# Optimization experiments

Hardware: AMD Instinct MI355X
Metric: run time of the kernel (lower is better)

Reference implementation:

```python
import jax, jax.numpy as jnp
import numpy as np

NUM_HEADS = 16
ROPE_THETA = 10000.0


def setup_inputs() -> dict:
    key = jax.random.key(0)
    k1, k2, k3 = jax.random.split(key, 3)
    B, S, D = 2, 2048, 1024
    std_qkv = float(np.sqrt(2.0 / (D + 3 * D)))
    std_out = float(np.sqrt(2.0 / (D + D)))
    return {
        "x": jax.random.normal(k1, (B, S, D), dtype=jnp.float32),
        "qkv_w": jax.random.normal(k2, (3 * D, D), dtype=jnp.float32) * std_qkv,
        "out_w": jax.random.normal(k3, (D, D), dtype=jnp.float32) * std_out,
        "token_positions": jnp.arange(S, dtype=jnp.int32),
    }


def _apply_rope(x, token_positions, theta=ROPE_THETA):
    # x: [B, H, S, d_k], token_positions: [S]
    d_k = x.shape[-1]
    inv_freqs = 1.0 / (theta ** (jnp.arange(0, d_k, 2, dtype=jnp.float32) / d_k))  # [d_k/2]
    angles = token_positions.astype(jnp.float32)[:, None] * inv_freqs[None, :]     # [S, d_k/2]
    cos, sin = jnp.cos(angles), jnp.sin(angles)
    x_even, x_odd = x[..., 0::2], x[..., 1::2]
    r_even = x_even * cos - x_odd * sin
    r_odd = x_even * sin + x_odd * cos
    # interleave back: [..., d_k/2, 2] -> [..., d_k]
    return jnp.stack([r_even, r_odd], axis=-1).reshape(x.shape)


def reference(x, qkv_w, out_w, token_positions):
    B, S, D = x.shape
    H = NUM_HEADS
    d_k = D // H

    qkv = jnp.einsum("bsd,ed->bse", x, qkv_w)                  # [B, S, 3*D]
    qkv = qkv.reshape(B, S, 3, H, d_k)
    q, k, v = (jnp.transpose(qkv[:, :, i], (0, 2, 1, 3)) for i in range(3))  # each [B, H, S, d_k]

    q = _apply_rope(q, token_positions)
    k = _apply_rope(k, token_positions)

    scale = 1.0 / jnp.sqrt(jnp.asarray(d_k, dtype=x.dtype))
    scores = jnp.einsum("bhqd,bhkd->bhqk", q, k) * scale       # [B, H, S, S]
    causal = jnp.tril(jnp.ones((S, S), dtype=bool))
    scores = jnp.where(causal, scores, jnp.asarray(-jnp.inf, dtype=scores.dtype))
    attn = jax.nn.softmax(scores, axis=-1)
    out = jnp.einsum("bhqk,bhkd->bhqd", attn, v)               # [B, H, S, d_k]
    out = jnp.transpose(out, (0, 2, 1, 3)).reshape(B, S, D)    # [B, S, D]
    return jnp.einsum("bsd,ed->bse", out, out_w)               # [B, S, D]
```

## Files before the change

### kernel.cpp

```cpp
#include <hip/hip_runtime.h>

typedef __bf16 bf16x8 __attribute__((ext_vector_type(8)));
typedef float f32x4 __attribute__((ext_vector_type(4)));
typedef unsigned short u16;
typedef u16 u16x8 __attribute__((ext_vector_type(8)));
typedef u16 u16x4 __attribute__((ext_vector_type(4)));
typedef u16 u16x2 __attribute__((ext_vector_type(2)));

__device__ __forceinline__ u16 f2bf(float f) {
    union { float f; unsigned u; } x; x.f = f;
    unsigned r = x.u + 0x7fffu + ((x.u >> 16) & 1u);
    return (u16)(r >> 16);
}
__device__ __forceinline__ float bf2f(u16 v) {
    union { unsigned u; float f; } x; x.u = ((unsigned)v) << 16;
    return x.f;
}
__device__ __forceinline__ bf16x8 as_bf16x8(u16x8 v) {
    return __builtin_bit_cast(bf16x8, v);
}
__device__ __forceinline__ void glds16(const void* g, void* l) {
    __builtin_amdgcn_global_load_lds(
        (const __attribute__((address_space(1))) void*)g,
        (__attribute__((address_space(3))) void*)l, 16, 0, 0);
}
__device__ __forceinline__ int swz(int r) { return (((r & 7) ^ ((r >> 3) & 7)) << 3); }

__global__ __launch_bounds__(256) void cvt3(const float* __restrict__ x,
                                            const float* __restrict__ w,
                                            const float* __restrict__ ow,
                                            u16* __restrict__ x16,
                                            u16* __restrict__ w16,
                                            u16* __restrict__ ow16) {
    int i = blockIdx.x * 256 + threadIdx.x;
    const float* in; u16* out; int off;
    if (i < 524288)       { in = x;  out = x16;  off = i; }
    else if (i < 917504)  { in = w;  out = w16;  off = i - 524288; }
    else                  { in = ow; out = ow16; off = i - 917504; }
    const float4* p = (const float4*)(in + (size_t)off * 8);
    float4 a = p[0], b = p[1];
    u16x8 o;
    o[0] = f2bf(a.x); o[1] = f2bf(a.y); o[2] = f2bf(a.z); o[3] = f2bf(a.w);
    o[4] = f2bf(b.x); o[5] = f2bf(b.y); o[6] = f2bf(b.z); o[7] = f2bf(b.w);
    *(u16x8*)(out + (size_t)off * 8) = o;
}

__global__ __launch_bounds__(256) void gemm_qkv(const u16* __restrict__ A,
                                                const u16* __restrict__ B,
                                                u16* __restrict__ Qb,
                                                u16* __restrict__ Kb,
                                                u16* __restrict__ Vt) {
    __shared__ u16 smem[17408];
    const int K = 1024, nbx = 24;
    const int tid = threadIdx.x, lane = tid & 63, wave = tid >> 6;
    const int cpx = gridDim.x >> 3;
    const int nid = (blockIdx.x & 7) * cpx + (blockIdx.x >> 3);
    const int m0 = (nid / nbx) << 7, n0 = (nid % nbx) << 7;
    const int wr = (wave >> 1) << 6, wc = (wave & 1) << 6;
    const int fr = lane & 15, fo = (lane >> 4) << 3;
    const int srow = tid >> 2, scol = (tid & 3) << 3;
    const u16* Ag = A + (size_t)(m0 + srow) * K + scol;
    const u16* Bg = B + (size_t)(n0 + srow) * K + scol;
    u16* AsW = smem + (wave << 9);
    u16* BsW = smem + 8192 + (wave << 9);
    f32x4 acc[4][4] = {};
    const int nsteps = K >> 5;
    glds16(Ag, AsW);
    glds16(Ag + (size_t)64 * K, AsW + 2048);
    glds16(Bg, BsW);
    glds16(Bg + (size_t)64 * K, BsW + 2048);
    int cur = 0;
    for (int s = 0; s < nsteps; ++s) {
        __syncthreads();
        if (s + 1 < nsteps) {
            const u16* Ap = Ag + (s + 1) * 32;
            const u16* Bp = Bg + (s + 1) * 32;
            const int nb = (cur ^ 1) << 12;
            glds16(Ap, AsW + nb);
            glds16(Ap + (size_t)64 * K, AsW + nb + 2048);
            glds16(Bp, BsW + nb);
            glds16(Bp + (size_t)64 * K, BsW + nb + 2048);
        }
        const u16* Ab = smem + (cur << 12);
        const u16* Bb = smem + 8192 + (cur << 12);
        bf16x8 af[4], bfr[4];
        #pragma unroll
        for (int i = 0; i < 4; ++i)
            af[i] = *(const bf16x8*)(Ab + (wr + i * 16 + fr) * 32 + fo);
        #pragma unroll
        for (int i = 0; i < 4; ++i)
            bfr[i] = *(const bf16x8*)(Bb + (wc + i * 16 + fr) * 32 + fo);
        #pragma unroll
        for (int i = 0; i < 4; ++i)
            #pragma unroll
            for (int j = 0; j < 4; ++j)
                acc[i][j] = __builtin_amdgcn_mfma_f32_16x16x32_bf16(af[i], bfr[j], acc[i][j], 0, 0, 0);
        cur ^= 1;
    }
    const int cr = (lane >> 4) << 2, cc = lane & 15;
    const int bb = m0 >> 11, sb = m0 & 2047;
    __syncthreads();
    if (n0 >= 2048) {
        #pragma unroll
        for (int i = 0; i < 4; ++i) {
            const int sl = wr + i * 16 + cr;
            const int k = sl & 63;
            const int p0 = ((sl >> 6) << 6) + ((k >> 5) << 5) + (((k >> 2) & 3) << 3)
                         + (((k >> 4) & 1) << 2);
            #pragma unroll
            for (int j = 0; j < 4; ++j) {
                const int c = wc + j * 16 + cc;
                u16x4 v4;
                #pragma unroll
                for (int r = 0; r < 4; ++r) v4[r] = f2bf(acc[i][j][r]);
                *(u16x4*)&smem[c * 136 + p0] = v4;
            }
        }
        __syncthreads();
        const int c = tid >> 1, hf = tid & 1;
        const int hh = c >> 6, d = c & 63;
        const int h0 = (n0 - 2048) >> 6;
        u16* dst = Vt + (((size_t)(bb * 16 + h0 + hh)) << 17) + ((size_t)d << 11)
                 + sb + (hf << 6);
        const u16* sr = &smem[c * 136 + (hf << 6)];
        #pragma unroll
        for (int q = 0; q < 8; ++q)
            *(u16x8*)(dst + q * 8) = *(const u16x8*)(sr + q * 8);
    } else {
        const bool isQ = (n0 < 1024);
        const float qs = isQ ? 0.18033688011112042f : 1.0f;
        const float sgn = (cc & 1) ? 1.f : -1.f;
        #pragma unroll
        for (int j = 0; j < 4; ++j) {
            const int c = wc + j * 16 + cc;
            const int tr = (c & 63) >> 1;
            const float invf = exp2f((float)tr * -0.4152410118609203f)
                             * 0.15915494309189535f;
            #pragma unroll
            for (int i = 0; i < 4; ++i) {
                #pragma unroll
                for (int r = 0; r < 4; ++r) {
                    const int sl = wr + i * 16 + cr + r;
                    float own  = acc[i][j][r];
                    float part = __shfl_xor(own, 1);
                    float rev  = (float)(sb + sl) * invf;
                    rev -= floorf(rev);
                    float sn = __builtin_amdgcn_sinf(rev);
                    float cs = __builtin_amdgcn_cosf(rev);
                    smem[sl * 136 + c] = f2bf((cs * own + sgn * sn * part) * qs);
                }
            }
        }
        __syncthreads();
        const int sl = tid >> 1, hh = tid & 1;
        const int h0 = (isQ ? n0 : (n0 - 1024)) >> 6;
        u16* Outb = isQ ? Qb : Kb;
        u16* dst = Outb + (((size_t)(bb * 16 + h0 + hh)) << 17)
                 + ((size_t)(sb + sl) << 6);
        const u16* sr = &smem[sl * 136 + (hh << 6)];
        #pragma unroll
        for (int q = 0; q < 8; ++q)
            *(u16x8*)(dst + q * 8) = *(const u16x8*)(sr + q * 8);
    }
}

template<bool BF16OUT>
__global__ __launch_bounds__(256) void gemm128(const u16* __restrict__ A,
                                               const u16* __restrict__ B,
                                               void* __restrict__ Cv,
                                               int N, int K, int nbx) {
    __shared__ u16 As[2][4096];
    __shared__ u16 Bs[2][4096];
    const int tid = threadIdx.x, lane = tid & 63, wave = tid >> 6;
    const int cpx = gridDim.x >> 3;
    const int nid = (blockIdx.x & 7) * cpx + (blockIdx.x >> 3);
    const int m0 = (nid / nbx) << 7, n0 = (nid % nbx) << 7;
    const int wr = (wave >> 1) << 6, wc = (wave & 1) << 6;
    const int fr = lane & 15, fo = (lane >> 4) << 3;
    const int srow = tid >> 2, scol = (tid & 3) << 3;
    const u16* Ag = A + (size_t)(m0 + srow) * K + scol;
    const u16* Bg = B + (size_t)(n0 + srow) * K + scol;
    u16* AsW = &As[0][0] + (wave << 9);
    u16* BsW = &Bs[0][0] + (wave << 9);
    f32x4 acc[4][4] = {};
    const int nsteps = K >> 5;
    glds16(Ag, AsW);
    glds16(Ag + (size_t)64 * K, AsW + 2048);
    glds16(Bg, BsW);
    glds16(Bg + (size_t)64 * K, BsW + 2048);
    int cur = 0;
    for (int s = 0; s < nsteps; ++s) {
        __syncthreads();
        if (s + 1 < nsteps) {
            const u16* Ap = Ag + (s + 1) * 32;
            const u16* Bp = Bg + (s + 1) * 32;
            const int nb = (cur ^ 1) << 12;
            glds16(Ap, AsW + nb);
            glds16(Ap + (size_t)64 * K, AsW + nb + 2048);
            glds16(Bp, BsW + nb);
            glds16(Bp + (size_t)64 * K, BsW + nb + 2048);
        }
        const u16* Ab = &As[cur][0];
        const u16* Bb = &Bs[cur][0];
        bf16x8 af[4], bfr[4];
        #pragma unroll
        for (int i = 0; i < 4; ++i)
            af[i] = *(const bf16x8*)(Ab + (wr + i * 16 + fr) * 32 + fo);
        #pragma unroll
        for (int i = 0; i < 4; ++i)
            bfr[i] = *(const bf16x8*)(Bb + (wc + i * 16 + fr) * 32 + fo);
        #pragma unroll
        for (int i = 0; i < 4; ++i)
            #pragma unroll
            for (int j = 0; j < 4; ++j)
                acc[i][j] = __builtin_amdgcn_mfma_f32_16x16x32_bf16(af[i], bfr[j], acc[i][j], 0, 0, 0);
        cur ^= 1;
    }
    const int cr = (lane >> 4) << 2, cc = lane & 15;
    if constexpr (BF16OUT) {
        u16* C = (u16*)Cv;
        #pragma unroll
        for (int i = 0; i < 4; ++i)
            for (int j = 0; j < 4; ++j)
                for (int r = 0; r < 4; ++r)
                    C[(size_t)(m0 + wr + i * 16 + cr + r) * N + (n0 + wc + j * 16 + cc)] =
                        f2bf(acc[i][j][r]);
    } else {
        float* C = (float*)Cv;
        #pragma unroll
        for (int i = 0; i < 4; ++i)
            for (int j = 0; j < 4; ++j)
                for (int r = 0; r < 4; ++r)
                    C[(size_t)(m0 + wr + i * 16 + cr + r) * N + (n0 + wc + j * 16 + cc)] =
                        acc[i][j][r];
    }
}

__global__ __launch_bounds__(512, 4) void attn_causal(const u16* __restrict__ Q,
                                                      const u16* __restrict__ K,
                                                      const u16* __restrict__ Vt,
                                                      u16* __restrict__ O) {
    __shared__ u16 smem[24576];
    __shared__ float cmb[5120];
    const int tid = threadIdx.x, lane = tid & 63, wave = tid >> 6;
    const int nid = ((blockIdx.x & 7) << 6) + (blockIdx.x >> 3);
    const int pr = nid & 15, h = (nid >> 4) & 15, b = nid >> 8;
    const int S = 2048;
    const size_t base = (size_t)((b << 4) + h) << 17;
    const int fr = lane & 15, fo = (lane >> 4) << 3, cr = (lane >> 4) << 2;
    const int schk = lane & 7, srow8 = lane >> 3;
    const int qsub = wave >> 1, half = wave & 1;
    float* const slot = cmb + qsub * 1280 + lane * 20;
    u16x8 ones_u;
    #pragma unroll
    for (int i = 0; i < 8; ++i) ones_u[i] = 0x3F80;
    const bf16x8 ones = as_bf16x8(ones_u);

    auto stage = [&](int t, int bi) {
        const int r  = (wave << 3) + srow8;
        const int ck = (schk ^ srow8 ^ wave) << 3;
        glds16(K  + base + ((size_t)((t << 6) + r) << 6) + ck,
               &smem[bi * 8192 + (wave << 9)]);
        glds16(Vt + base + ((size_t)r << 11) + (t << 6) + ck,
               &smem[bi * 8192 + 4096 + (wave << 9)]);
    };

    for (int phase = 0; phase < 2; ++phase) {
        const int qt = phase ? (31 - pr) : pr;
        const int nkt = qt + 1;
        const int qw = (qt << 6) + (qsub << 4);
        bf16x8 aq0, aq1;
        {
            const u16* qrow = Q + base + (size_t)(qw + fr) * 64;
            aq0 = as_bf16x8(*(const u16x8*)(qrow + fo));
            aq1 = as_bf16x8(*(const u16x8*)(qrow + 32 + fo));
        }
        f32x4 oacc[4] = {};
        f32x4 lacc = {};
        const int qloc = (qsub << 4) + fr;
        stage(0, 0);
        if (nkt > 1) stage(1, 1);
        int cur = 0;
        for (int t = 0; t < nkt; ++t) {
            if (t + 1 < nkt) asm volatile("s_waitcnt vmcnt(2)" ::: "memory");
            else             asm volatile("s_waitcnt vmcnt(0)" ::: "memory");
            __builtin_amdgcn_s_barrier();
            __builtin_amdgcn_sched_barrier(0);
            int nb = cur + 2; if (nb >= 3) nb -= 3;
            if (t + 2 < nkt) stage(t + 2, nb);
            const u16* Kb = smem + cur * 8192;
            const u16* Vb = smem + cur * 8192 + 4096;
            const bool diag = (t == nkt - 1);
            f32x4 sacc[2];
            __builtin_amdgcn_s_setprio(1);
            #pragma unroll
            for (int ch = 0; ch < 2; ++ch) {
                const int r = ((half << 1) + ch) * 16 + fr;
                const int sw = swz(r);
                bf16x8 bk0 = *(const bf16x8*)&Kb[r * 64 + (fo ^ sw)];
                bf16x8 bk1 = *(const bf16x8*)&Kb[r * 64 + ((32 + fo) ^ sw)];
                f32x4 sc = {};
                sc = __builtin_amdgcn_mfma_f32_16x16x32_bf16(bk0, aq0, sc, 0, 0, 0);
                sc = __builtin_amdgcn_mfma_f32_16x16x32_bf16(bk1, aq1, sc, 0, 0, 0);
                sacc[ch] = sc;
            }
            __builtin_amdgcn_s_setprio(0);
            bf16x8 pa;
            #pragma unroll
            for (int ch = 0; ch < 2; ++ch) {
                const int cglob = (half << 1) + ch;
                #pragma unroll
                for (int r = 0; r < 4; ++r) {
                    float e = exp2f(sacc[ch][r]);
                    if (diag) {
                        const int kloc = (cglob << 4) + cr + r;
                        e = (kloc <= qloc) ? e : 0.f;
                    }
                    pa[ch * 4 + r] = (__bf16)e;
                }
            }
            __builtin_amdgcn_s_setprio(1);
            lacc = __builtin_amdgcn_mfma_f32_16x16x32_bf16(pa, ones, lacc, 0, 0, 0);
            #pragma unroll
            for (int tt = 0; tt < 4; ++tt) {
                const int d = tt * 16 + fr;
                bf16x8 bv = *(const bf16x8*)&Vb[d * 64 + (((half << 5) + fo) ^ swz(d))];
                oacc[tt] = __builtin_amdgcn_mfma_f32_16x16x32_bf16(pa, bv, oacc[tt], 0, 0, 0);
            }
            __builtin_amdgcn_s_setprio(0);
            cur = (cur + 1 == 3) ? 0 : cur + 1;
        }
        __syncthreads();
        if (half) {
            #pragma unroll
            for (int tt = 0; tt < 4; ++tt) *(f32x4*)(slot + tt * 4) = oacc[tt];
            *(f32x4*)(slot + 16) = lacc;
        }
        __syncthreads();
        if (!half) {
            #pragma unroll
            for (int tt = 0; tt < 4; ++tt) oacc[tt] += *(const f32x4*)(slot + tt * 4);
            lacc += *(const f32x4*)(slot + 16);
            f32x4 inv;
            #pragma unroll
            for (int j = 0; j < 4; ++j) inv[j] = 1.f / lacc[j];
            #pragma unroll
            for (int tt = 0; tt < 4; ++tt)
                for (int j = 0; j < 4; ++j)
                    O[(size_t)(b * S + qw + cr + j) * 1024 + h * 64 + tt * 16 + fr] =
                        f2bf(oacc[tt][j] * inv[j]);
        }
        __syncthreads();
    }
}

extern "C" void kernel_launch(void* const* d_in, const int* in_sizes, int n_in,
                              void* d_out, int out_size, void* d_ws, size_t ws_size,
                              hipStream_t stream) {
    const float* x     = (const float*)d_in[0];
    const float* qkv_w = (const float*)d_in[1];
    const float* out_w = (const float*)d_in[2];
    float* out = (float*)d_out;

    char* ws = (char*)d_ws;
    u16* Qb    = (u16*)(ws + 25165824);
    u16* Kb    = (u16*)(ws + 33554432);
    u16* Vtg   = (u16*)(ws + 41943040);
    u16* x16   = (u16*)(ws + 50331648);
    u16* att16 = (u16*)(ws + 50331648);
    u16* w16   = (u16*)(ws + 58720256);
    u16* ow16  = (u16*)(ws + 65011712);

    cvt3<<<4096, 256, 0, stream>>>(x, qkv_w, out_w, x16, w16, ow16);
    gemm_qkv<<<768, 256, 0, stream>>>(x16, w16, Qb, Kb, Vtg);
    attn_causal<<<512, 512, 0, stream>>>(Qb, Kb, Vtg, att16);
    gemm128<false><<<256, 256, 0, stream>>>(att16, ow16, (void*)out, 1024, 1024, 8);
}
```

Before: 115.4 us.

## Switch attention to 32x32x16 MFMA with 4 waves and 32-row query tiles

Rewrites the causal attention inner loop to use 32x32x16 bf16 MFMA instead of 16x16x32. Each block now runs 4 waves (256 threads, two per query half), each wave covering 32 query rows and 32 keys, and K/V staging is widened to two loads per wave. The larger MFMA tile is meant to cut LDS operand reads per flop and issue overhead. In exchange it needs more accumulator registers, does a two-step LDS reduction of the output, and changes the V-transpose store permutation in the QKV GEMM epilogue, which could break the layout if it does not match the new reads.

Result: slower. 118.8 us (+2.9%).

```diff
diff --git a/kernel.cpp b/kernel.cpp
--- a/kernel.cpp
+++ b/kernel.cpp
@@ -2,19 +2,15 @@
 
 typedef __bf16 bf16x8 __attribute__((ext_vector_type(8)));
 typedef float f32x4 __attribute__((ext_vector_type(4)));
+typedef float f32x16 __attribute__((ext_vector_type(16)));
 typedef unsigned short u16;
 typedef u16 u16x8 __attribute__((ext_vector_type(8)));
 typedef u16 u16x4 __attribute__((ext_vector_type(4)));
-typedef u16 u16x2 __attribute__((ext_vector_type(2)));
 
 __device__ __forceinline__ u16 f2bf(float f) {
     union { float f; unsigned u; } x; x.f = f;
     unsigned r = x.u + 0x7fffu + ((x.u >> 16) & 1u);
     return (u16)(r >> 16);
-}
-__device__ __forceinline__ float bf2f(u16 v) {
-    union { unsigned u; float f; } x; x.u = ((unsigned)v) << 16;
-    return x.f;
 }
 __device__ __forceinline__ bf16x8 as_bf16x8(u16x8 v) {
     return __builtin_bit_cast(bf16x8, v);
@@ -105,16 +101,19 @@
         for (int i = 0; i < 4; ++i) {
             const int sl = wr + i * 16 + cr;
             const int k = sl & 63;
-            const int p0 = ((sl >> 6) << 6) + ((k >> 5) << 5) + (((k >> 2) & 3) << 3)
-                         + (((k >> 4) & 1) << 2);
+            const int p0 = ((sl >> 6) << 6)
+                         + (k & ~12) | 0;
+            const int ps = (((sl >> 6) << 6) + (k & ~12))
+                         + ((cr & 4) << 1) + ((cr & 8) >> 1);
             #pragma unroll
             for (int j = 0; j < 4; ++j) {
                 const int c = wc + j * 16 + cc;
                 u16x4 v4;
                 #pragma unroll
                 for (int r = 0; r < 4; ++r) v4[r] = f2bf(acc[i][j][r]);
-                *(u16x4*)&smem[c * 136 + p0] = v4;
-            }
+                *(u16x4*)&smem[c * 136 + ps] = v4;
+            }
+            (void)p0;
         }
         __syncthreads();
         const int c = tid >> 1, hf = tid & 1;
@@ -164,10 +163,9 @@
     }
 }
 
-template<bool BF16OUT>
 __global__ __launch_bounds__(256) void gemm128(const u16* __restrict__ A,
                                                const u16* __restrict__ B,
-                                               void* __restrict__ Cv,
+                                               float* __restrict__ C,
                                                int N, int K, int nbx) {
     __shared__ u16 As[2][4096];
     __shared__ u16 Bs[2][4096];
@@ -217,138 +215,157 @@
         cur ^= 1;
     }
     const int cr = (lane >> 4) << 2, cc = lane & 15;
-    if constexpr (BF16OUT) {
-        u16* C = (u16*)Cv;
-        #pragma unroll
-        for (int i = 0; i < 4; ++i)
-            for (int j = 0; j < 4; ++j)
-                for (int r = 0; r < 4; ++r)
-                    C[(size_t)(m0 + wr + i * 16 + cr + r) * N + (n0 + wc + j * 16 + cc)] =
-                        f2bf(acc[i][j][r]);
-    } else {
-        float* C = (float*)Cv;
-        #pragma unroll
-        for (int i = 0; i < 4; ++i)
-            for (int j = 0; j < 4; ++j)
-                for (int r = 0; r < 4; ++r)
-                    C[(size_t)(m0 + wr + i * 16 + cr + r) * N + (n0 + wc + j * 16 + cc)] =
-                        acc[i][j][r];
-    }
-}
-
-__global__ __launch_bounds__(512, 4) void attn_causal(const u16* __restrict__ Q,
+    #pragma unroll
+    for (int i = 0; i < 4; ++i)
+        for (int j = 0; j < 4; ++j)
+            for (int r = 0; r < 4; ++r)
+                C[(size_t)(m0 + wr + i * 16 + cr + r) * N + (n0 + wc + j * 16 + cc)] =
+                    acc[i][j][r];
+}
+
+__global__ __launch_bounds__(256, 2) void attn_causal(const u16* __restrict__ Q,
                                                       const u16* __restrict__ K,
                                                       const u16* __restrict__ Vt,
                                                       u16* __restrict__ O) {
     __shared__ u16 smem[24576];
-    __shared__ float cmb[5120];
+    __shared__ float cmb[4224];
     const int tid = threadIdx.x, lane = tid & 63, wave = tid >> 6;
     const int nid = ((blockIdx.x & 7) << 6) + (blockIdx.x >> 3);
     const int pr = nid & 15, h = (nid >> 4) & 15, b = nid >> 8;
-    const int S = 2048;
     const size_t base = (size_t)((b << 4) + h) << 17;
-    const int fr = lane & 15, fo = (lane >> 4) << 3, cr = (lane >> 4) << 2;
+    const int lq = lane & 31, hi = lane >> 5;
     const int schk = lane & 7, srow8 = lane >> 3;
-    const int qsub = wave >> 1, half = wave & 1;
-    float* const slot = cmb + qsub * 1280 + lane * 20;
+    const int qh = wave >> 1, kh = wave & 1;
+    float* const slot = cmb + (qh * 64 + lane) * 33;
     u16x8 ones_u;
     #pragma unroll
     for (int i = 0; i < 8; ++i) ones_u[i] = 0x3F80;
     const bf16x8 ones = as_bf16x8(ones_u);
 
     auto stage = [&](int t, int bi) {
-        const int r  = (wave << 3) + srow8;
-        const int ck = (schk ^ srow8 ^ wave) << 3;
-        glds16(K  + base + ((size_t)((t << 6) + r) << 6) + ck,
-               &smem[bi * 8192 + (wave << 9)]);
-        glds16(Vt + base + ((size_t)r << 11) + (t << 6) + ck,
-               &smem[bi * 8192 + 4096 + (wave << 9)]);
+        #pragma unroll
+        for (int g = 0; g < 2; ++g) {
+            const int rg = (wave << 4) + (g << 3);
+            const int r  = rg + srow8;
+            const int ck = (schk ^ srow8 ^ ((2 * wave + g) & 7)) << 3;
+            glds16(K  + base + ((size_t)((t << 6) + r) << 6) + ck,
+                   &smem[bi * 8192 + (rg << 6)]);
+            glds16(Vt + base + ((size_t)r << 11) + (t << 6) + ck,
+                   &smem[bi * 8192 + 4096 + (rg << 6)]);
+        }
     };
 
     for (int phase = 0; phase < 2; ++phase) {
         const int qt = phase ? (31 - pr) : pr;
         const int nkt = qt + 1;
-        const int qw = (qt << 6) + (qsub << 4);
-        bf16x8 aq0, aq1;
+        const int qw = (qt << 6) + (qh << 5);
+        const int qg = qw + lq;
+        bf16x8 aq[4];
         {
-            const u16* qrow = Q + base + (size_t)(qw + fr) * 64;
-            aq0 = as_bf16x8(*(const u16x8*)(qrow + fo));
-            aq1 = as_bf16x8(*(const u16x8*)(qrow + 32 + fo));
-        }
-        f32x4 oacc[4] = {};
-        f32x4 lacc = {};
-        const int qloc = (qsub << 4) + fr;
+            const u16* qrow = Q + base + ((size_t)qg << 6) + (hi << 3);
+            #pragma unroll
+            for (int m = 0; m < 4; ++m)
+                aq[m] = as_bf16x8(*(const u16x8*)(qrow + m * 16));
+        }
+        f32x16 oacc0 = {}, oacc1 = {}, lacc = {};
         stage(0, 0);
         if (nkt > 1) stage(1, 1);
         int cur = 0;
         for (int t = 0; t < nkt; ++t) {
-            if (t + 1 < nkt) asm volatile("s_waitcnt vmcnt(2)" ::: "memory");
+            if (t + 1 < nkt) asm volatile("s_waitcnt vmcnt(4)" ::: "memory");
             else             asm volatile("s_waitcnt vmcnt(0)" ::: "memory");
             __builtin_amdgcn_s_barrier();
             __builtin_amdgcn_sched_barrier(0);
             int nb = cur + 2; if (nb >= 3) nb -= 3;
             if (t + 2 < nkt) stage(t + 2, nb);
             const u16* Kb = smem + cur * 8192;
-            const u16* Vb = smem + cur * 8192 + 4096;
+            const u16* Vb = Kb + 4096;
             const bool diag = (t == nkt - 1);
-            f32x4 sacc[2];
+            f32x16 sacc = {};
             __builtin_amdgcn_s_setprio(1);
-            #pragma unroll
-            for (int ch = 0; ch < 2; ++ch) {
-                const int r = ((half << 1) + ch) * 16 + fr;
-                const int sw = swz(r);
-                bf16x8 bk0 = *(const bf16x8*)&Kb[r * 64 + (fo ^ sw)];
-                bf16x8 bk1 = *(const bf16x8*)&Kb[r * 64 + ((32 + fo) ^ sw)];
-                f32x4 sc = {};
-                sc = __builtin_amdgcn_mfma_f32_16x16x32_bf16(bk0, aq0, sc, 0, 0, 0);
-                sc = __builtin_amdgcn_mfma_f32_16x16x32_bf16(bk1, aq1, sc, 0, 0, 0);
-                sacc[ch] = sc;
+            {
+                const int krow = (kh << 5) + lq;
+                const int sw = swz(krow);
+                #pragma unroll
+                for (int m = 0; m < 4; ++m) {
+                    bf16x8 bk = *(const bf16x8*)&Kb[krow * 64 +
+                                                    (((m << 4) + (hi << 3)) ^ sw)];
+                    sacc = __builtin_amdgcn_mfma_f32_32x32x16_bf16(bk, aq[m], sacc, 0, 0, 0);
+                }
             }
             __builtin_amdgcn_s_setprio(0);
-            bf16x8 pa;
-            #pragma unroll
-            for (int ch = 0; ch < 2; ++ch) {
-                const int cglob = (half << 1) + ch;
-                #pragma unroll
-                for (int r = 0; r < 4; ++r) {
-                    float e = exp2f(sacc[ch][r]);
-                    if (diag) {
-                        const int kloc = (cglob << 4) + cr + r;
-                        e = (kloc <= qloc) ? e : 0.f;
-                    }
-                    pa[ch * 4 + r] = (__bf16)e;
-                }
+            bf16x8 pa0, pa1;
+            #pragma unroll
+            for (int r = 0; r < 8; ++r) {
+                float e = exp2f(sacc[r]);
+                if (diag) {
+                    const int kgl = (t << 6) + (kh << 5) + (r & 3) + ((r >> 2) << 3) + (hi << 2);
+                    e = (kgl <= qg) ? e : 0.f;
+                }
+                pa0[r] = (__bf16)e;
+            }
+            #pragma unroll
+            for (int r = 0; r < 8; ++r) {
+                float e = exp2f(sacc[8 + r]);
+                if (diag) {
+                    const int kgl = (t << 6) + (kh << 5) + 16 + (r & 3) + ((r >> 2) << 3) + (hi << 2);
+                    e = (kgl <= qg) ? e : 0.f;
+                }
+                pa1[r] = (__bf16)e;
             }
             __builtin_amdgcn_s_setprio(1);
-            lacc = __builtin_amdgcn_mfma_f32_16x16x32_bf16(pa, ones, lacc, 0, 0, 0);
-            #pragma unroll
-            for (int tt = 0; tt < 4; ++tt) {
-                const int d = tt * 16 + fr;
-                bf16x8 bv = *(const bf16x8*)&Vb[d * 64 + (((half << 5) + fo) ^ swz(d))];
-                oacc[tt] = __builtin_amdgcn_mfma_f32_16x16x32_bf16(pa, bv, oacc[tt], 0, 0, 0);
+            lacc = __builtin_amdgcn_mfma_f32_32x32x16_bf16(pa0, ones, lacc, 0, 0, 0);
+            lacc = __builtin_amdgcn_mfma_f32_32x32x16_bf16(pa1, ones, lacc, 0, 0, 0);
+            #pragma unroll
+            for (int dn = 0; dn < 2; ++dn) {
+                const int vrow = (dn << 5) + lq;
+                const int sw = swz(vrow);
+                bf16x8 bv0 = *(const bf16x8*)&Vb[vrow * 64 +
+                                                 (((kh << 5) + (hi << 3)) ^ sw)];
+                bf16x8 bv1 = *(const bf16x8*)&Vb[vrow * 64 +
+                                                 (((kh << 5) + 16 + (hi << 3)) ^ sw)];
+                if (dn == 0) {
+                    oacc0 = __builtin_amdgcn_mfma_f32_32x32x16_bf16(pa0, bv0, oacc0, 0, 0, 0);
+                    oacc0 = __builtin_amdgcn_mfma_f32_32x32x16_bf16(pa1, bv1, oacc0, 0, 0, 0);
+                } else {
+                    oacc1 = __builtin_amdgcn_mfma_f32_32x32x16_bf16(pa0, bv0, oacc1, 0, 0, 0);
+                    oacc1 = __builtin_amdgcn_mfma_f32_32x32x16_bf16(pa1, bv1, oacc1, 0, 0, 0);
+                }
             }
             __builtin_amdgcn_s_setprio(0);
             cur = (cur + 1 == 3) ? 0 : cur + 1;
         }
         __syncthreads();
-        if (half) {
-            #pragma unroll
-            for (int tt = 0; tt < 4; ++tt) *(f32x4*)(slot + tt * 4) = oacc[tt];
-            *(f32x4*)(slot + 16) = lacc;
-        }
-        __syncthreads();
-        if (!half) {
-            #pragma unroll
-            for (int tt = 0; tt < 4; ++tt) oacc[tt] += *(const f32x4*)(slot + tt * 4);
-            lacc += *(const f32x4*)(slot + 16);
-            f32x4 inv;
-            #pragma unroll
-            for (int j = 0; j < 4; ++j) inv[j] = 1.f / lacc[j];
-            #pragma unroll
-            for (int tt = 0; tt < 4; ++tt)
-                for (int j = 0; j < 4; ++j)
-                    O[(size_t)(b * S + qw + cr + j) * 1024 + h * 64 + tt * 16 + fr] =
-                        f2bf(oacc[tt][j] * inv[j]);
+        if (kh) {
+            #pragma unroll
+            for (int r = 0; r < 16; ++r) slot[r] = oacc0[r];
+            #pragma unroll
+            for (int r = 0; r < 16; ++r) slot[16 + r] = lacc[r];
+        }
+        __syncthreads();
+        if (!kh) {
+            #pragma unroll
+            for (int r = 0; r < 16; ++r) oacc0[r] += slot[r];
+            #pragma unroll
+            for (int r = 0; r < 16; ++r) lacc[r] += slot[16 + r];
+        }
+        __syncthreads();
+        if (kh) {
+            #pragma unroll
+            for (int r = 0; r < 16; ++r) slot[r] = oacc1[r];
+        }
+        __syncthreads();
+        if (!kh) {
+            #pragma unroll
+            for (int r = 0; r < 16; ++r) oacc1[r] += slot[r];
+            #pragma unroll
+            for (int r = 0; r < 16; ++r) {
+                const int q = qw + (r & 3) + ((r >> 2) << 3) + (hi << 2);
+                const float iv = 1.f / lacc[r];
+                u16* op = O + ((size_t)((b << 11) + q) << 10) + (h << 6) + lq;
+                op[0]  = f2bf(oacc0[r] * iv);
+                op[32] = f2bf(oacc1[r] * iv);
+            }
         }
         __syncthreads();
     }
@@ -373,6 +390,6 @@
 
     cvt3<<<4096, 256, 0, stream>>>(x, qkv_w, out_w, x16, w16, ow16);
     gemm_qkv<<<768, 256, 0, stream>>>(x16, w16, Qb, Kb, Vtg);
-    attn_causal<<<512, 512, 0, stream>>>(Qb, Kb, Vtg, att16);
-    gemm128<false><<<256, 256, 0, stream>>>(att16, ow16, (void*)out, 1024, 1024, 8);
-}
+    attn_causal<<<512, 256, 0, stream>>>(Qb, Kb, Vtg, att16);
+    gemm128<<<256, 256, 0, stream>>>(att16, ow16, out, 1024, 1024, 8);
+}
```
